# Kernel tuning notes

Measured on AMD Instinct MI355X. Metric: run time of the kernel, lower is better.

The kernel has to match this reference:

```python
import jax, jax.numpy as jnp
import numpy as np

D_MODEL = 1024
N_HEADS = 16
HEAD_DIM = D_MODEL // N_HEADS


def setup_inputs() -> dict:
    key = jax.random.key(0)
    ks = jax.random.split(key, 9)
    B, S = 4, 2048
    x = jax.random.normal(ks[0], (B, S, D_MODEL), dtype=jnp.float32)
    init = 1.0 / np.sqrt(D_MODEL)
    def lin(kw, kb):
        W = jax.random.uniform(kw, (D_MODEL, D_MODEL), jnp.float32, -init, init)
        b = jax.random.uniform(kb, (D_MODEL,), jnp.float32, -init, init)
        return W, b
    Wq, bq = lin(ks[1], ks[2])
    Wk, bk = lin(ks[3], ks[4])
    Wv, bv = lin(ks[5], ks[6])
    Wo, bo = lin(ks[7], ks[8])
    return {"x": x, "Wq": Wq, "bq": bq, "Wk": Wk, "bk": bk,
            "Wv": Wv, "bv": bv, "Wo": Wo, "bo": bo}


def reference(x, Wq, bq, Wk, bk, Wv, bv, Wo, bo):
    B, S, _ = x.shape
    scale = jnp.sqrt(jnp.float32(HEAD_DIM))
    def split_heads(t):  # [B,S,D] -> [B,H,S,hd]
        return t.reshape(B, S, N_HEADS, HEAD_DIM).transpose(0, 2, 1, 3)
    q = split_heads(x @ Wq.T + bq)
    k = split_heads(x @ Wk.T + bk)
    v = split_heads(x @ Wv.T + bv)
    attn = jnp.einsum('bhqd,bhkd->bhqk', q, k) / scale
    attn = jax.nn.softmax(attn, axis=-1)
    out = jnp.einsum('bhqk,bhkd->bhqd', attn, v)  # [B,H,S,hd]
    out = out.transpose(0, 2, 1, 3).reshape(B, S, D_MODEL)
    return out @ Wo.T + bo
```

## Files before the change

kernel.cpp:

```cpp
#include <hip/hip_runtime.h>
#include <hip/hip_bf16.h>
#include <stdint.h>

typedef __attribute__((ext_vector_type(8))) short bf16x8;
typedef __attribute__((ext_vector_type(4))) float f32x4;
typedef __attribute__((ext_vector_type(16))) float f32x16;
typedef __attribute__((ext_vector_type(2))) unsigned int u32x2;
typedef unsigned short u16;

#define DEVI static __device__ __forceinline__

DEVI u16 f2bf(float f) {
  union { float f; uint32_t u; } x; x.f = f;
  uint32_t r = (x.u + 0x7FFFu + ((x.u >> 16) & 1u)) >> 16;
  return (u16)r;
}

DEVI void gload_lds16(const void* g, void* lds) {
  __builtin_amdgcn_global_load_lds(
      (const __attribute__((address_space(1))) void*)(void*)g,
      (__attribute__((address_space(3))) void*)lds, 16, 0, 0);
}

DEVI unsigned ldsaddr(const void* p) { return (unsigned)(uintptr_t)p; }

__global__ void cvt_all_kernel(const float* __restrict__ x,
                               const float* __restrict__ Wq, const float* __restrict__ Wk,
                               const float* __restrict__ Wv, const float* __restrict__ Wo,
                               const float* __restrict__ bq, const float* __restrict__ bk,
                               const float* __restrict__ bv,
                               u16* __restrict__ xb, u16* __restrict__ Wqkvb,
                               u16* __restrict__ Wob, float* __restrict__ bqkv) {
  const int X4 = 2097152;
  const int W4 = 262144;
  const int total = X4 + 4 * W4 + 768;
  int i = blockIdx.x * blockDim.x + threadIdx.x;
  const int stride = gridDim.x * blockDim.x;
  for (; i < total; i += stride) {
    if (i < X4) {
      float4 v = ((const float4*)x)[i];
      ((ushort4*)xb)[i] = make_ushort4(f2bf(v.x), f2bf(v.y), f2bf(v.z), f2bf(v.w));
    } else if (i < X4 + 4 * W4) {
      int j = i - X4;
      int which = j >> 18;
      int o = j & (W4 - 1);
      const float* src = which == 0 ? Wq : which == 1 ? Wk : which == 2 ? Wv : Wo;
      u16* dst = (which == 3) ? Wob : (Wqkvb + (size_t)which * 1048576);
      float4 v = ((const float4*)src)[o];
      ((ushort4*)dst)[o] = make_ushort4(f2bf(v.x), f2bf(v.y), f2bf(v.z), f2bf(v.w));
    } else {
      int j = i - X4 - 4 * W4;
      int which = j >> 8;
      int o = j & 255;
      const float* src = which == 0 ? bq : which == 1 ? bk : bv;
      ((float4*)bqkv)[which * 256 + o] = ((const float4*)src)[o];
    }
  }
}

template<int OUT_BF16>
__global__ __launch_bounds__(512, 2)
void gemm_bt8_kernel(const u16* __restrict__ A, const u16* __restrict__ B,
                     const float* __restrict__ bias, void* __restrict__ C,
                     int M, int N, int K, int scale_cols, float scale_val) {
  __shared__ u16 As[2][8192];
  __shared__ u16 Bs[2][16384];
  const int tid = threadIdx.x;
  const int l = tid & 63;
  const int w = tid >> 6;
  const int wm = w >> 2, wn = w & 3;
  const int bn = blockIdx.x, bm = blockIdx.y;

  const int trow = tid >> 3;
  const int lc = (tid & 7) ^ (trow & 7);
  const u16* gA0 = A + (size_t)(bm * 128 + trow) * K + lc * 8;
  const u16* gA1 = gA0 + (size_t)64 * K;
  const u16* gB0 = B + (size_t)(bn * 256 + trow) * K + lc * 8;
  const u16* gB1 = gB0 + (size_t)64 * K;
  const u16* gB2 = gB0 + (size_t)128 * K;
  const u16* gB3 = gB0 + (size_t)192 * K;

#define GSTAGE(d, kt) { \
    const size_t ko = (size_t)(kt) * 64; \
    gload_lds16(gA0 + ko, &As[d][tid * 8]); \
    gload_lds16(gA1 + ko, &As[d][4096 + tid * 8]); \
    gload_lds16(gB0 + ko, &Bs[d][tid * 8]); \
    gload_lds16(gB1 + ko, &Bs[d][4096 + tid * 8]); \
    gload_lds16(gB2 + ko, &Bs[d][8192 + tid * 8]); \
    gload_lds16(gB3 + ko, &Bs[d][12288 + tid * 8]); \
  }

  const int arow = (wm * 64 + (l & 15)) * 64;
  const int brow = (wn * 64 + (l & 15)) * 64;
  int coff[2];
#pragma unroll
  for (int kk = 0; kk < 2; ++kk) coff[kk] = (((kk * 4 + (l >> 4)) ^ (l & 7)) * 8);

  f32x4 acc[4][4] = {};
  const int NT = K >> 6;

  GSTAGE(0, 0);

  for (int kt = 0; kt < NT; ++kt) {
    const int cur = kt & 1;
    asm volatile("s_waitcnt vmcnt(0)" ::: "memory");
    __builtin_amdgcn_s_barrier();
    asm volatile("" ::: "memory");
    if (kt < NT - 1) GSTAGE(cur ^ 1, kt + 1);

    const u16* ap = &As[cur][0];
    const u16* bp = &Bs[cur][0];

    bf16x8 bf[4][2], af[2];
#pragma unroll
    for (int nf = 0; nf < 4; ++nf)
#pragma unroll
      for (int kk = 0; kk < 2; ++kk)
        bf[nf][kk] = *(const bf16x8*)&bp[brow + nf * 1024 + coff[kk]];
#pragma unroll
    for (int kk = 0; kk < 2; ++kk) af[kk] = *(const bf16x8*)&ap[arow + coff[kk]];
    asm volatile("s_waitcnt lgkmcnt(0)" ::: "memory");
    __builtin_amdgcn_sched_barrier(0);
    __builtin_amdgcn_s_setprio(1);
#pragma unroll
    for (int kk = 0; kk < 2; ++kk)
#pragma unroll
      for (int nf = 0; nf < 4; ++nf)
        acc[0][nf] = __builtin_amdgcn_mfma_f32_16x16x32_bf16(af[kk], bf[nf][kk], acc[0][nf], 0, 0, 0);
    __builtin_amdgcn_s_setprio(0);
    __builtin_amdgcn_s_barrier();

#pragma unroll
    for (int mf = 1; mf < 4; ++mf) {
#pragma unroll
      for (int kk = 0; kk < 2; ++kk)
        af[kk] = *(const bf16x8*)&ap[arow + mf * 1024 + coff[kk]];
      asm volatile("s_waitcnt lgkmcnt(0)" ::: "memory");
      __builtin_amdgcn_sched_barrier(0);
      __builtin_amdgcn_s_setprio(1);
#pragma unroll
      for (int kk = 0; kk < 2; ++kk)
#pragma unroll
        for (int nf = 0; nf < 4; ++nf)
          acc[mf][nf] = __builtin_amdgcn_mfma_f32_16x16x32_bf16(af[kk], bf[nf][kk], acc[mf][nf], 0, 0, 0);
      __builtin_amdgcn_s_setprio(0);
      if (mf < 3) __builtin_amdgcn_s_barrier();
    }
    asm volatile("" ::: "memory");
  }

  const int rbase = bm * 128 + wm * 64 + (l >> 4) * 4;
  const int cbase = bn * 256 + wn * 64 + (l & 15);
#pragma unroll
  for (int nf = 0; nf < 4; ++nf) {
    int col = cbase + nf * 16;
    float bsv = bias[col];
    float sc = (col < scale_cols) ? scale_val : 1.0f;
#pragma unroll
    for (int mf = 0; mf < 4; ++mf) {
#pragma unroll
      for (int j = 0; j < 4; ++j) {
        int row = rbase + mf * 16 + j;
        float v = (acc[mf][nf][j] + bsv) * sc;
        if (OUT_BF16) ((u16*)C)[(size_t)row * N + col] = f2bf(v);
        else          ((float*)C)[(size_t)row * N + col] = v;
      }
    }
  }
#undef GSTAGE
}

DEVI void softmax_pa(f32x16& sA, f32x16& sB, bf16x8* pa, float& lsum, int hi) {
  float rs = 0.f;
#pragma unroll
  for (int r = 0; r < 16; ++r) { sA[r] = __builtin_amdgcn_exp2f(sA[r]); rs += sA[r]; }
#pragma unroll
  for (int r = 0; r < 16; ++r) { sB[r] = __builtin_amdgcn_exp2f(sB[r]); rs += sB[r]; }
  lsum += rs + __shfl_xor(rs, 32, 64);
#pragma unroll
  for (int i = 0; i < 4; ++i) {
    float p0 = (8 * i + 0 < 16) ? sA[(8 * i + 0) & 15] : sB[(8 * i + 0) & 15];
    float p1 = (8 * i + 1 < 16) ? sA[(8 * i + 1) & 15] : sB[(8 * i + 1) & 15];
    float p2 = (8 * i + 2 < 16) ? sA[(8 * i + 2) & 15] : sB[(8 * i + 2) & 15];
    float p3 = (8 * i + 3 < 16) ? sA[(8 * i + 3) & 15] : sB[(8 * i + 3) & 15];
    float p4 = (8 * i + 4 < 16) ? sA[(8 * i + 4) & 15] : sB[(8 * i + 4) & 15];
    float p5 = (8 * i + 5 < 16) ? sA[(8 * i + 5) & 15] : sB[(8 * i + 5) & 15];
    float p6 = (8 * i + 6 < 16) ? sA[(8 * i + 6) & 15] : sB[(8 * i + 6) & 15];
    float p7 = (8 * i + 7 < 16) ? sA[(8 * i + 7) & 15] : sB[(8 * i + 7) & 15];
    unsigned a0, a1, b0, b1;
    asm("v_cvt_pk_bf16_f32 %0, %1, %2" : "=v"(a0) : "v"(p0), "v"(p1));
    asm("v_cvt_pk_bf16_f32 %0, %1, %2" : "=v"(a1) : "v"(p2), "v"(p3));
    asm("v_cvt_pk_bf16_f32 %0, %1, %2" : "=v"(b0) : "v"(p4), "v"(p5));
    asm("v_cvt_pk_bf16_f32 %0, %1, %2" : "=v"(b1) : "v"(p6), "v"(p7));
    unsigned t0 = hi ? a0 : b0;
    unsigned t1 = hi ? a1 : b1;
    unsigned x0 = (unsigned)__shfl_xor((int)t0, 32, 64);
    unsigned x1 = (unsigned)__shfl_xor((int)t1, 32, 64);
    union { unsigned u[4]; bf16x8 v; } U;
    U.u[0] = hi ? x0 : a0;
    U.u[1] = hi ? x1 : a1;
    U.u[2] = hi ? b0 : x0;
    U.u[3] = hi ? b1 : x1;
    pa[i] = U.v;
  }
}

__global__ __launch_bounds__(256, 2)
void attn_kernel(const u16* __restrict__ QKV, u16* __restrict__ O) {
  __shared__ u16 Ks[3][4096];
  __shared__ u16 Vs[3][4096];

  const int tid = threadIdx.x;
  const int l = tid & 63, w = tid >> 6;
  const int hi = l >> 5, c = l & 31;
  const int bh = blockIdx.y, b = bh >> 4, h = bh & 15;
  const int qb = blockIdx.x * 256 + w * 64;
  const size_t rowbase = (size_t)b * 2048;

  bf16x8 qf0[4], qf1[4];
  {
    const u16* Qp0 = QKV + (rowbase + qb + c) * 3072 + h * 64 + hi * 8;
    const u16* Qp1 = QKV + (rowbase + qb + 32 + c) * 3072 + h * 64 + hi * 8;
#pragma unroll
    for (int kk = 0; kk < 4; ++kk) {
      qf0[kk] = *(const bf16x8*)(Qp0 + kk * 16);
      qf1[kk] = *(const bf16x8*)(Qp1 + kk * 16);
    }
  }

  const int kd0 = (w * 2 + 0) * 64 + l;
  const int kd1 = (w * 2 + 1) * 64 + l;
  const int rK0 = kd0 >> 3, dbK0 = (kd0 & 7) ^ (rK0 & 7);
  const int rK1 = kd1 >> 3, dbK1 = (kd1 & 7) ^ (rK1 & 7);
  const u16* srcK0 = QKV + (rowbase + rK0) * 3072 + 1024 + h * 64 + dbK0 * 8;
  const u16* srcK1 = QKV + (rowbase + rK1) * 3072 + 1024 + h * 64 + dbK1 * 8;
  const int kV0 = (kd0 >> 5) * 4 + ((kd0 >> 1) & 3), dV0 = ((kd0 >> 3) & 3) * 16 + (kd0 & 1) * 8;
  const int kV1 = (kd1 >> 5) * 4 + ((kd1 >> 1) & 3), dV1 = ((kd1 >> 3) & 3) * 16 + (kd1 & 1) * 8;
  const u16* srcV0 = QKV + (rowbase + kV0) * 3072 + 2048 + h * 64 + dV0;
  const u16* srcV1 = QKV + (rowbase + kV1) * 3072 + 2048 + h * 64 + dV1;

#define STAGE(buf, tile) { \
    const size_t koff = (size_t)(tile) * 64 * 3072; \
    gload_lds16(srcK0 + koff, &Ks[buf][(w * 2 + 0) * 512]); \
    gload_lds16(srcK1 + koff, &Ks[buf][(w * 2 + 1) * 512]); \
    gload_lds16(srcV0 + koff, &Vs[buf][(w * 2 + 0) * 512]); \
    gload_lds16(srcV1 + koff, &Vs[buf][(w * 2 + 1) * 512]); \
  }

  int koffs[4];
#pragma unroll
  for (int kk = 0; kk < 4; ++kk) koffs[kk] = (((kk * 2 + hi) ^ (c & 7)) * 8);
  const int kbase = c * 64;

  const unsigned vbase = ldsaddr(&Vs[0][0]) + (unsigned)(hi * 1024 + (c >> 4) * 128 + (c & 15) * 8);

  f32x16 o00 = {0,0,0,0,0,0,0,0,0,0,0,0,0,0,0,0};
  f32x16 o01 = {0,0,0,0,0,0,0,0,0,0,0,0,0,0,0,0};
  f32x16 o10 = {0,0,0,0,0,0,0,0,0,0,0,0,0,0,0,0};
  f32x16 o11 = {0,0,0,0,0,0,0,0,0,0,0,0,0,0,0,0};
  float lsum0 = 0.f, lsum1 = 0.f;

  STAGE(0, 0);
  STAGE(1, 1);

  int cur = 0;
  for (int t = 0; t < 32; ++t) {
    if (t < 31) { asm volatile("s_waitcnt vmcnt(4)" ::: "memory"); }
    else        { asm volatile("s_waitcnt vmcnt(0)" ::: "memory"); }
    __builtin_amdgcn_s_barrier();
    asm volatile("" ::: "memory");

    if (t < 30) {
      int bs = cur + 2; if (bs >= 3) bs -= 3;
      STAGE(bs, t + 2);
    }

    const u16* kp = &Ks[cur][0];
    bf16x8 kf[2][4];
#pragma unroll
    for (int kb = 0; kb < 2; ++kb)
#pragma unroll
      for (int kk = 0; kk < 4; ++kk)
        kf[kb][kk] = *(const bf16x8*)&kp[kbase + kb * 2048 + koffs[kk]];

    f32x16 sA0 = {0,0,0,0,0,0,0,0,0,0,0,0,0,0,0,0};
    f32x16 sB0 = {0,0,0,0,0,0,0,0,0,0,0,0,0,0,0,0};
    f32x16 sA1 = {0,0,0,0,0,0,0,0,0,0,0,0,0,0,0,0};
    f32x16 sB1 = {0,0,0,0,0,0,0,0,0,0,0,0,0,0,0,0};
#pragma unroll
    for (int kk = 0; kk < 4; ++kk) {
      sA0 = __builtin_amdgcn_mfma_f32_32x32x16_bf16(kf[0][kk], qf0[kk], sA0, 0, 0, 0);
      sB0 = __builtin_amdgcn_mfma_f32_32x32x16_bf16(kf[1][kk], qf0[kk], sB0, 0, 0, 0);
      sA1 = __builtin_amdgcn_mfma_f32_32x32x16_bf16(kf[0][kk], qf1[kk], sA1, 0, 0, 0);
      sB1 = __builtin_amdgcn_mfma_f32_32x32x16_bf16(kf[1][kk], qf1[kk], sB1, 0, 0, 0);
    }

    const unsigned va = vbase + (unsigned)(cur * 8192);
    u32x2 tt[4][4];
#pragma unroll
    for (int ks = 0; ks < 4; ++ks) {
      unsigned va_ks = va + (unsigned)(ks * 2048);
      asm volatile("ds_read_b64_tr_b16 %0, %1 offset:0"   : "=v"(tt[ks][0]) : "v"(va_ks));
      asm volatile("ds_read_b64_tr_b16 %0, %1 offset:512" : "=v"(tt[ks][1]) : "v"(va_ks));
      asm volatile("ds_read_b64_tr_b16 %0, %1 offset:256" : "=v"(tt[ks][2]) : "v"(va_ks));
      asm volatile("ds_read_b64_tr_b16 %0, %1 offset:768" : "=v"(tt[ks][3]) : "v"(va_ks));
    }

    bf16x8 pa0[4];
    softmax_pa(sA0, sB0, pa0, lsum0, hi);

    asm volatile("s_waitcnt lgkmcnt(0)" ::: "memory");
    __builtin_amdgcn_sched_barrier(0);

#pragma unroll
    for (int ks = 0; ks < 4; ++ks) {
      union { u32x2 d2[2]; bf16x8 v; } V0, V1;
      V0.d2[0] = tt[ks][0]; V0.d2[1] = tt[ks][1];
      V1.d2[0] = tt[ks][2]; V1.d2[1] = tt[ks][3];
      o00 = __builtin_amdgcn_mfma_f32_32x32x16_bf16(pa0[ks], V0.v, o00, 0, 0, 0);
      o01 = __builtin_amdgcn_mfma_f32_32x32x16_bf16(pa0[ks], V1.v, o01, 0, 0, 0);
    }

    bf16x8 pa1[4];
    softmax_pa(sA1, sB1, pa1, lsum1, hi);

#pragma unroll
    for (int ks = 0; ks < 4; ++ks) {
      union { u32x2 d2[2]; bf16x8 v; } V0, V1;
      V0.d2[0] = tt[ks][0]; V0.d2[1] = tt[ks][1];
      V1.d2[0] = tt[ks][2]; V1.d2[1] = tt[ks][3];
      o10 = __builtin_amdgcn_mfma_f32_32x32x16_bf16(pa1[ks], V0.v, o10, 0, 0, 0);
      o11 = __builtin_amdgcn_mfma_f32_32x32x16_bf16(pa1[ks], V1.v, o11, 0, 0, 0);
    }

    asm volatile("" ::: "memory");
    cur = (cur == 2) ? 0 : cur + 1;
  }

  u16* Op0 = O + (rowbase + qb) * 1024 + h * 64 + c;
  u16* Op1 = O + (rowbase + qb + 32) * 1024 + h * 64 + c;
#pragma unroll
  for (int r = 0; r < 16; ++r) {
    int q = (r & 3) + 8 * (r >> 2) + 4 * hi;
    float inv0 = 1.0f / __shfl(lsum0, q, 64);
    float inv1 = 1.0f / __shfl(lsum1, q, 64);
    Op0[(size_t)q * 1024]      = f2bf(o00[r] * inv0);
    Op0[(size_t)q * 1024 + 32] = f2bf(o01[r] * inv0);
    Op1[(size_t)q * 1024]      = f2bf(o10[r] * inv1);
    Op1[(size_t)q * 1024 + 32] = f2bf(o11[r] * inv1);
  }
#undef STAGE
}

extern "C" void kernel_launch(void* const* d_in, const int* in_sizes, int n_in,
                              void* d_out, int out_size, void* d_ws, size_t ws_size,
                              hipStream_t stream) {
  const float* x  = (const float*)d_in[0];
  const float* Wq = (const float*)d_in[1];
  const float* bq = (const float*)d_in[2];
  const float* Wk = (const float*)d_in[3];
  const float* bk = (const float*)d_in[4];
  const float* Wv = (const float*)d_in[5];
  const float* bv = (const float*)d_in[6];
  const float* Wo = (const float*)d_in[7];
  const float* bo = (const float*)d_in[8];
  float* out = (float*)d_out;

  char* ws = (char*)d_ws;
  u16*   xb    = (u16*)(ws);
  u16*   Wqkvb = (u16*)(ws + 16777216);
  u16*   Wob   = (u16*)(ws + 23068672);
  float* bqkv  = (float*)(ws + 25165824);
  u16*   QKV   = (u16*)(ws + 25178112);
  u16*   Oa    = (u16*)(ws + 75509760);

  cvt_all_kernel<<<2048, 256, 0, stream>>>(x, Wq, Wk, Wv, Wo, bq, bk, bv,
                                           xb, Wqkvb, Wob, bqkv);

  gemm_bt8_kernel<1><<<dim3(12, 64), 512, 0, stream>>>(xb, Wqkvb, bqkv, QKV,
                                                       8192, 3072, 1024, 1024,
                                                       0.125f * 1.4426950408889634f);
  attn_kernel<<<dim3(8, 64), 256, 0, stream>>>(QKV, Oa);
  gemm_bt8_kernel<0><<<dim3(4, 64), 512, 0, stream>>>(Oa, Wob, bo, out,
                                                      8192, 1024, 1024, 0, 1.0f);
}
```

Measured before the change: 213.9 us.

## Split GEMM K-tile into half-stages with deeper async prefetch pipeline

Restructures the bf16 GEMM so each 64-wide K tile is loaded as two 32-wide halves into a unified LDS buffer. Half-stage loads are issued ahead with partial vmcnt waits, keeping up to two half-stages in flight instead of draining all loads each iteration. The LDS layout drops the XOR swizzle in favour of 32-element rows. The main loop now computes all 16 MFMAs per half-stage instead of interleaving barriers per M fragment. Risks are LDS bank conflicts from the unswizzled layout and redundant clamped loads at the tail.

```diff
diff --git a/kernel.cpp b/kernel.cpp
--- a/kernel.cpp
+++ b/kernel.cpp
@@ -60,91 +60,85 @@
 
 template<int OUT_BF16>
 __global__ __launch_bounds__(512, 2)
-void gemm_bt8_kernel(const u16* __restrict__ A, const u16* __restrict__ B,
-                     const float* __restrict__ bias, void* __restrict__ C,
-                     int M, int N, int K, int scale_cols, float scale_val) {
-  __shared__ u16 As[2][8192];
-  __shared__ u16 Bs[2][16384];
+void gemm_kh_kernel(const u16* __restrict__ A, const u16* __restrict__ B,
+                    const float* __restrict__ bias, void* __restrict__ C,
+                    int M, int N, int K, int scale_cols, float scale_val) {
+  __shared__ u16 S[49152];
   const int tid = threadIdx.x;
   const int l = tid & 63;
   const int w = tid >> 6;
   const int wm = w >> 2, wn = w & 3;
   const int bn = blockIdx.x, bm = blockIdx.y;
 
-  const int trow = tid >> 3;
-  const int lc = (tid & 7) ^ (trow & 7);
-  const u16* gA0 = A + (size_t)(bm * 128 + trow) * K + lc * 8;
-  const u16* gA1 = gA0 + (size_t)64 * K;
-  const u16* gB0 = B + (size_t)(bn * 256 + trow) * K + lc * 8;
-  const u16* gB1 = gB0 + (size_t)64 * K;
-  const u16* gB2 = gB0 + (size_t)128 * K;
-  const u16* gB3 = gB0 + (size_t)192 * K;
-
-#define GSTAGE(d, kt) { \
-    const size_t ko = (size_t)(kt) * 64; \
-    gload_lds16(gA0 + ko, &As[d][tid * 8]); \
-    gload_lds16(gA1 + ko, &As[d][4096 + tid * 8]); \
-    gload_lds16(gB0 + ko, &Bs[d][tid * 8]); \
-    gload_lds16(gB1 + ko, &Bs[d][4096 + tid * 8]); \
-    gload_lds16(gB2 + ko, &Bs[d][8192 + tid * 8]); \
-    gload_lds16(gB3 + ko, &Bs[d][12288 + tid * 8]); \
-  }
-
-  const int arow = (wm * 64 + (l & 15)) * 64;
-  const int brow = (wn * 64 + (l & 15)) * 64;
-  int coff[2];
-#pragma unroll
-  for (int kk = 0; kk < 2; ++kk) coff[kk] = (((kk * 4 + (l >> 4)) ^ (l & 7)) * 8);
+  const u16* sA  = A + (size_t)(bm * 128 + (tid >> 2)) * K + (tid & 3) * 8;
+  const u16* sB0 = B + (size_t)(bn * 256 + (tid >> 2)) * K + (tid & 3) * 8;
+  const u16* sB1 = sB0 + (size_t)128 * K;
+
+#define QSTAGE(bufi, kh, ko) { \
+    gload_lds16(sA  + (ko), &S[(bufi) * 24576 + (kh) * 4096 + tid * 8]); \
+    gload_lds16(sB0 + (ko), &S[(bufi) * 24576 + 8192 + (kh) * 8192 + tid * 8]); \
+    gload_lds16(sB1 + (ko), &S[(bufi) * 24576 + 8192 + (kh) * 8192 + 4096 + tid * 8]); \
+  }
+
+  const int arow = (wm * 64 + (l & 15)) * 32 + (l >> 4) * 8;
+  const int brow = (wn * 64 + (l & 15)) * 32 + (l >> 4) * 8;
 
   f32x4 acc[4][4] = {};
   const int NT = K >> 6;
 
-  GSTAGE(0, 0);
+  QSTAGE(0, 0, 0);
+  QSTAGE(0, 1, 32);
+  QSTAGE(1, 0, 64);
 
   for (int kt = 0; kt < NT; ++kt) {
-    const int cur = kt & 1;
-    asm volatile("s_waitcnt vmcnt(0)" ::: "memory");
+    const int bufo = (kt & 1) * 24576;
+
+    asm volatile("s_waitcnt vmcnt(6)" ::: "memory");
     __builtin_amdgcn_s_barrier();
     asm volatile("" ::: "memory");
-    if (kt < NT - 1) GSTAGE(cur ^ 1, kt + 1);
-
-    const u16* ap = &As[cur][0];
-    const u16* bp = &Bs[cur][0];
-
-    bf16x8 bf[4][2], af[2];
-#pragma unroll
-    for (int nf = 0; nf < 4; ++nf)
-#pragma unroll
-      for (int kk = 0; kk < 2; ++kk)
-        bf[nf][kk] = *(const bf16x8*)&bp[brow + nf * 1024 + coff[kk]];
-#pragma unroll
-    for (int kk = 0; kk < 2; ++kk) af[kk] = *(const bf16x8*)&ap[arow + coff[kk]];
-    asm volatile("s_waitcnt lgkmcnt(0)" ::: "memory");
-    __builtin_amdgcn_sched_barrier(0);
-    __builtin_amdgcn_s_setprio(1);
-#pragma unroll
-    for (int kk = 0; kk < 2; ++kk)
-#pragma unroll
-      for (int nf = 0; nf < 4; ++nf)
-        acc[0][nf] = __builtin_amdgcn_mfma_f32_16x16x32_bf16(af[kk], bf[nf][kk], acc[0][nf], 0, 0, 0);
-    __builtin_amdgcn_s_setprio(0);
-    __builtin_amdgcn_s_barrier();
-
-#pragma unroll
-    for (int mf = 1; mf < 4; ++mf) {
-#pragma unroll
-      for (int kk = 0; kk < 2; ++kk)
-        af[kk] = *(const bf16x8*)&ap[arow + mf * 1024 + coff[kk]];
+    { int ts = (kt + 1 < NT) ? kt + 1 : NT - 1;
+      QSTAGE((kt + 1) & 1, 1, ts * 64 + 32); }
+    {
+      const u16* ap = &S[bufo];
+      const u16* bp = &S[bufo + 8192];
+      bf16x8 af[4], bf[4];
+#pragma unroll
+      for (int mf = 0; mf < 4; ++mf) af[mf] = *(const bf16x8*)&ap[arow + mf * 512];
+#pragma unroll
+      for (int nf = 0; nf < 4; ++nf) bf[nf] = *(const bf16x8*)&bp[brow + nf * 512];
       asm volatile("s_waitcnt lgkmcnt(0)" ::: "memory");
       __builtin_amdgcn_sched_barrier(0);
       __builtin_amdgcn_s_setprio(1);
 #pragma unroll
-      for (int kk = 0; kk < 2; ++kk)
+      for (int mf = 0; mf < 4; ++mf)
 #pragma unroll
         for (int nf = 0; nf < 4; ++nf)
-          acc[mf][nf] = __builtin_amdgcn_mfma_f32_16x16x32_bf16(af[kk], bf[nf][kk], acc[mf][nf], 0, 0, 0);
+          acc[mf][nf] = __builtin_amdgcn_mfma_f32_16x16x32_bf16(af[mf], bf[nf], acc[mf][nf], 0, 0, 0);
       __builtin_amdgcn_s_setprio(0);
-      if (mf < 3) __builtin_amdgcn_s_barrier();
+    }
+
+    asm volatile("s_waitcnt vmcnt(6)" ::: "memory");
+    __builtin_amdgcn_s_barrier();
+    asm volatile("" ::: "memory");
+    { int ts = (kt + 2 < NT) ? kt + 2 : NT - 1;
+      QSTAGE(kt & 1, 0, ts * 64); }
+    {
+      const u16* ap = &S[bufo + 4096];
+      const u16* bp = &S[bufo + 8192 + 8192];
+      bf16x8 af[4], bf[4];
+#pragma unroll
+      for (int mf = 0; mf < 4; ++mf) af[mf] = *(const bf16x8*)&ap[arow + mf * 512];
+#pragma unroll
+      for (int nf = 0; nf < 4; ++nf) bf[nf] = *(const bf16x8*)&bp[brow + nf * 512];
+      asm volatile("s_waitcnt lgkmcnt(0)" ::: "memory");
+      __builtin_amdgcn_sched_barrier(0);
+      __builtin_amdgcn_s_setprio(1);
+#pragma unroll
+      for (int mf = 0; mf < 4; ++mf)
+#pragma unroll
+        for (int nf = 0; nf < 4; ++nf)
+          acc[mf][nf] = __builtin_amdgcn_mfma_f32_16x16x32_bf16(af[mf], bf[nf], acc[mf][nf], 0, 0, 0);
+      __builtin_amdgcn_s_setprio(0);
     }
     asm volatile("" ::: "memory");
   }
@@ -167,7 +161,7 @@
       }
     }
   }
-#undef GSTAGE
+#undef QSTAGE
 }
 
 DEVI void softmax_pa(f32x16& sA, f32x16& sB, bf16x8* pa, float& lsum, int hi) {
@@ -377,10 +371,10 @@
   cvt_all_kernel<<<2048, 256, 0, stream>>>(x, Wq, Wk, Wv, Wo, bq, bk, bv,
                                            xb, Wqkvb, Wob, bqkv);
 
-  gemm_bt8_kernel<1><<<dim3(12, 64), 512, 0, stream>>>(xb, Wqkvb, bqkv, QKV,
-                                                       8192, 3072, 1024, 1024,
-                                                       0.125f * 1.4426950408889634f);
+  gemm_kh_kernel<1><<<dim3(12, 64), 512, 0, stream>>>(xb, Wqkvb, bqkv, QKV,
+                                                      8192, 3072, 1024, 1024,
+                                                      0.125f * 1.4426950408889634f);
   attn_kernel<<<dim3(8, 64), 256, 0, stream>>>(QKV, Oa);
-  gemm_bt8_kernel<0><<<dim3(4, 64), 512, 0, stream>>>(Oa, Wob, bo, out,
-                                                      8192, 1024, 1024, 0, 1.0f);
-}
+  gemm_kh_kernel<0><<<dim3(4, 64), 512, 0, stream>>>(Oa, Wob, bo, out,
+                                                     8192, 1024, 1024, 0, 1.0f);
+}
```

New measurement: 191.3 us. -10.6%, faster.
